# Kernel tuning notes

Hardware: AMD Instinct MI355X
Metric: run time of the kernel (lower is better)

Reference implementation:

```python
import math
import jax, jax.numpy as jnp
import numpy as np

B, T, D, NE, DS, H = 8, 1024, 768, 8, 128, 64
ROUTE_TEMP = 1.0


def setup_inputs() -> dict:
    key = jax.random.key(0)
    ks = jax.random.split(key, 32)
    rn = lambda k, shape, s=0.02: (jax.random.normal(k, shape, jnp.float32) * s)
    inp = {
        "h_seq": jax.random.normal(ks[0], (B, T, D), jnp.float32),
        "entity_keys": rn(ks[1], (NE, D)),
        "state0": rn(ks[2], (NE, DS)),
        # input_proj
        "Wi": rn(ks[3], (DS, D), 0.05), "bi": jnp.zeros((DS,), jnp.float32),
        # GRUCell (torch layout: [3*DS, DS], gate order r,z,n)
        "W_ih": rn(ks[4], (3 * DS, DS), 0.05), "W_hh": rn(ks[5], (3 * DS, DS), 0.05),
        "b_ih": rn(ks[6], (3 * DS,), 0.05), "b_hh": rn(ks[7], (3 * DS,), 0.05),
        # memory_proj
        "Wm": rn(ks[8], (D, DS), 0.05), "bm": jnp.zeros((D,), jnp.float32),
        # sequence_proj
        "Ws": rn(ks[9], (D, NE * D), 0.02), "bs": jnp.zeros((D,), jnp.float32),
        # heads: Linear(DS,H) -> GELU -> Linear(H,1)
        "Wh1": rn(ks[10], (H, DS), 0.05), "bh1": jnp.zeros((H,), jnp.float32),
        "Wh2": rn(ks[11], (1, H), 0.05), "bh2": jnp.zeros((1,), jnp.float32),
        "Wt1": rn(ks[12], (H, DS), 0.05), "bt1": jnp.zeros((H,), jnp.float32),
        "Wt2": rn(ks[13], (1, H), 0.05), "bt2": jnp.zeros((1,), jnp.float32),
        "Wv1": rn(ks[14], (H, DS), 0.05), "bv1": jnp.zeros((H,), jnp.float32),
        "Wv2": rn(ks[15], (1, H), 0.05), "bv2": jnp.zeros((1,), jnp.float32),
    }
    return inp


def _gru_cell(x, h, W_ih, W_hh, b_ih, b_hh):
    # x, h: [..., DS]; torch GRUCell semantics, gate order (r, z, n)
    gi = x @ W_ih.T + b_ih
    gh = h @ W_hh.T + b_hh
    i_r, i_z, i_n = jnp.split(gi, 3, axis=-1)
    h_r, h_z, h_n = jnp.split(gh, 3, axis=-1)
    r = jax.nn.sigmoid(i_r + h_r)
    z = jax.nn.sigmoid(i_z + h_z)
    n = jnp.tanh(i_n + r * h_n)
    return (1.0 - z) * n + z * h


def _head(s, W1, b1, W2, b2):
    # s: [B,T,NE,DS] -> logits [B,T,NE]
    hdn = jax.nn.gelu(s @ W1.T + b1, approximate=False)
    return (hdn @ W2.T + b2)[..., 0]


def reference(h_seq, entity_keys, state0, Wi, bi, W_ih, W_hh, b_ih, b_hh,
              Wm, bm, Ws, bs, Wh1, bh1, Wh2, bh2, Wt1, bt1, Wt2, bt2,
              Wv1, bv1, Wv2, bv2):
    scale = math.sqrt(D) * max(1e-4, ROUTE_TEMP)
    route_logits = jnp.einsum("btd,ed->bte", h_seq, entity_keys) / scale
    route_weights = jax.nn.softmax(route_logits, axis=-1)           # [B,T,NE]
    projected = h_seq @ Wi.T + bi                                   # [B,T,DS]
    routed = route_weights[..., None] * projected[:, :, None, :]    # [B,T,NE,DS]

    def step(state, x_t):  # state,x_t: [B,NE,DS]
        new = _gru_cell(x_t, state, W_ih, W_hh, b_ih, b_hh)
        return new, new

    init = jnp.broadcast_to(state0, (B, NE, DS))
    _, states = jax.lax.scan(step, init, routed.transpose(1, 0, 2, 3))
    state_stack = states.transpose(1, 0, 2, 3)                      # [B,T,NE,DS]

    memory_stack = state_stack @ Wm.T + bm                          # [B,T,NE,D]
    holder = _head(state_stack, Wh1, bh1, Wh2, bh2)
    tagged = _head(state_stack, Wt1, bt1, Wt2, bt2)
    visible = _head(state_stack, Wv1, bv1, Wv2, bv2)
    pooled = memory_stack.reshape(B, T, NE * D) @ Ws.T + bs         # [B,T,D]
    return pooled, memory_stack, state_stack, holder, tagged, visible, route_weights
```

## Files before the change

### kernel.cpp

```cpp
#include <hip/hip_runtime.h>
#include <hip/hip_bf16.h>

typedef unsigned short u16;
typedef unsigned int u32;
typedef __bf16 bf16x8 __attribute__((ext_vector_type(8)));
typedef float f32x4 __attribute__((ext_vector_type(4)));

#define OUT_POOLED 0
#define OUT_MEM    6291456
#define OUT_STATE  56623104
#define OUT_HOLD   65011712
#define OUT_ROUTE  65208320

#define SW(r) (((r)&7)<<4)

__device__ __forceinline__ float b2f(u16 u){ u32 v=((u32)u)<<16; float f; __builtin_memcpy(&f,&v,4); return f; }
__device__ __forceinline__ u16 f2b(float f){ __hip_bfloat16 h=__float2bfloat16(f); u16 r; __builtin_memcpy(&r,&h,2); return r; }
__device__ __forceinline__ float sigf(float x){ return __builtin_amdgcn_rcpf(1.0f+__builtin_amdgcn_exp2f(-1.4426950408889634f*x)); }
__device__ __forceinline__ float tanh_(float x){ return 1.0f-2.0f*__builtin_amdgcn_rcpf(1.0f+__builtin_amdgcn_exp2f(2.8853900817779268f*x)); }
__device__ __forceinline__ float geluf(float x){
  float z = 0.7071067811865476f*x;
  float az = __builtin_fabsf(z);
  float t = __builtin_amdgcn_rcpf(1.0f+0.3275911f*az);
  float p = t*(0.254829592f+t*(-0.284496736f+t*(1.421413741f+t*(-1.453152027f+t*1.061405429f))));
  float e = __builtin_amdgcn_exp2f(-1.4426950408889634f*az*az);
  float er = 1.0f-p*e;
  er = (z<0.0f)? -er : er;
  return 0.5f*x*(1.0f+er);
}

__global__ void k_prep(const float* __restrict__ Ws, const float* __restrict__ bs,
                       const float* __restrict__ bm, const float* __restrict__ Wm,
                       const float* __restrict__ Wh1, const float* __restrict__ bh1,
                       const float* __restrict__ Wt1, const float* __restrict__ bt1,
                       const float* __restrict__ Wv1, const float* __restrict__ bv1,
                       const float* __restrict__ Wi, const float* __restrict__ ek,
                       const float* __restrict__ Wih,
                       u16* __restrict__ wcat, float* __restrict__ bcat, float* __restrict__ bcomb,
                       u16* __restrict__ wib2, u16* __restrict__ wihb, u16* __restrict__ wmT)
{
  __shared__ float bmS[768];
  int tid = threadIdx.x;
  for(int i=tid;i<768;i+=256) bmS[i]=bm[i];
  __syncthreads();
  {
    int w = tid>>6, lane = tid&63;
    int d = blockIdx.x*4 + w;
    float acc=0.f;
    for(int e=0;e<8;e++){
      const float* row = Ws + (size_t)d*6144 + e*768;
      #pragma unroll
      for(int it=0; it<3; it++){
        int c = it*256 + lane*4;
        float4 u = *reinterpret_cast<const float4*>(row + c);
        acc += u.x*bmS[c]+u.y*bmS[c+1]+u.z*bmS[c+2]+u.w*bmS[c+3];
      }
    }
    #pragma unroll
    for(int o=32;o>0;o>>=1) acc += __shfl_down(acc,o);
    if(lane==0) bcomb[d]=bs[d]+acc;
  }
  for(int idx = blockIdx.x*256+tid; idx<381888; idx += gridDim.x*256){
    if(idx<960){
      int n=idx;
      float v;
      if(n<768) v=bm[n];
      else { int j=n-768; v = (j<64)? bh1[j] : (j<128)? bt1[j-64] : bv1[j-128]; }
      bcat[n]=v;
    } else if(idx<123840){
      int c=idx-960; int n=c>>7, k=c&127;
      float v;
      if(n<768) v=Wm[n*128+k];
      else if(n<832) v=Wh1[(n-768)*128+k];
      else if(n<896) v=Wt1[(n-832)*128+k];
      else v=Wv1[(n-896)*128+k];
      wcat[c]=f2b(v);
    } else if(idx<234432){
      int j=idx-123840; int r=j/768, k=j-r*768;
      float v = (r<128)? Wi[r*768+k] : (r<136)? ek[(r-128)*768+k] : 0.f;
      wib2[j]=f2b(v);
    } else if(idx<283584){
      int j=idx-234432;
      wihb[j]=f2b(Wih[j]);
    } else {
      int j=idx-283584; int s=j/768, d2=j-s*768;
      wmT[j]=f2b(Wm[d2*128+s]);
    }
  }
}

__global__ __launch_bounds__(256,2) void k_wcomb(const float* __restrict__ Ws, const u16* __restrict__ wmT,
                                                 u16* __restrict__ wcomb)
{
  __shared__ u16 AsU[128*104];
  __shared__ u16 BsU[128*104];
  char* AsB=(char*)AsU; char* BsB=(char*)BsU;
  int tid=threadIdx.x;
  int dt=blockIdx.x, e=blockIdx.y;
  int d0=dt*128;
  int w=tid>>6, L=tid&63, q4=L>>4, il=L&15;
  int msub=w*32;
  const f32x4 fz={0.f,0.f,0.f,0.f};
  f32x4 acc[2][8];
  #pragma unroll
  for(int tm=0;tm<2;tm++)
    #pragma unroll
    for(int tn=0;tn<8;tn++) acc[tm][tn]=fz;
  for(int kc=0;kc<8;kc++){
    __syncthreads();
    for(int it=0;it<12;it++){
      int slot=it*256+tid; int r=slot/24, c4=(slot-r*24)*4;
      float4 u=*reinterpret_cast<const float4*>(Ws + (size_t)(d0+r)*6144 + e*768 + kc*96 + c4);
      u16 v[4]={f2b(u.x),f2b(u.y),f2b(u.z),f2b(u.w)};
      uint2 p; __builtin_memcpy(&p,v,8);
      *reinterpret_cast<uint2*>(AsB + r*208 + c4*2) = p;
    }
    for(int it=0;it<6;it++){
      int slot=it*256+tid; int r=slot/12, o8=(slot-r*12)*8;
      uint4 u=*reinterpret_cast<const uint4*>(wmT + (size_t)r*768 + kc*96 + o8);
      *reinterpret_cast<uint4*>(BsB + r*208 + o8*2) = u;
    }
    __syncthreads();
    #pragma unroll
    for(int kt=0;kt<3;kt++){
      int kb=(kt*32+q4*8)*2;
      bf16x8 a0=__builtin_bit_cast(bf16x8,*reinterpret_cast<const uint4*>(AsB + (msub+il)*208 + kb));
      bf16x8 a1=__builtin_bit_cast(bf16x8,*reinterpret_cast<const uint4*>(AsB + (msub+16+il)*208 + kb));
      #pragma unroll
      for(int tn=0;tn<8;tn++){
        bf16x8 b=__builtin_bit_cast(bf16x8,*reinterpret_cast<const uint4*>(BsB + (tn*16+il)*208 + kb));
        acc[0][tn]=__builtin_amdgcn_mfma_f32_16x16x32_bf16(a0,b,acc[0][tn],0,0,0);
        acc[1][tn]=__builtin_amdgcn_mfma_f32_16x16x32_bf16(a1,b,acc[1][tn],0,0,0);
      }
    }
  }
  #pragma unroll
  for(int tm=0;tm<2;tm++){
    #pragma unroll
    for(int tn=0;tn<8;tn++){
      #pragma unroll
      for(int i=0;i<4;i++){
        int d=d0+msub+tm*16+q4*4+i;
        wcomb[d*1024 + e*128 + tn*16+il]=f2b(acc[tm][tn][i]);
      }
    }
  }
}

__global__ __launch_bounds__(256,2) void k_route(const float* __restrict__ hseq,
                                                 const u16* __restrict__ wib2, const u16* __restrict__ wihb,
                                                 const float* __restrict__ bi,
                                                 const float* __restrict__ bih, const float* __restrict__ bhh,
                                                 u16* __restrict__ gpre, float* __restrict__ out)
{
  __shared__ u16 AsU[16*768];
  __shared__ u16 BsU[15360];
  __shared__ u16 prS[16*128];
  __shared__ float lgs[16][8];
  __shared__ float wSm[16][8];
  __shared__ float biS[128];
  __shared__ float bS[384];
  char* AsB=(char*)AsU; char* BsB=(char*)BsU; char* prB=(char*)prS;
  int tid=threadIdx.x;
  int row0=blockIdx.x*16;
  {
    int r=tid>>4, c0=(tid&15)*48;
    const float* src=hseq+(size_t)(row0+r)*768+c0;
    #pragma unroll
    for(int m=0;m<12;m++){
      float4 u=*reinterpret_cast<const float4*>(src+m*4);
      u16 v[4]={f2b(u.x),f2b(u.y),f2b(u.z),f2b(u.w)};
      uint2 p; __builtin_memcpy(&p,v,8);
      int k=c0+m*4;
      *reinterpret_cast<uint2*>(AsB + r*1536 + ((k*2)^SW(r))) = p;
    }
  }
  if(tid<32){ *reinterpret_cast<float4*>(&biS[tid*4]) = *reinterpret_cast<const float4*>(bi+tid*4); }
  if(tid>=64&&tid<160){
    int j4=(tid-64)*4;
    float4 u=*reinterpret_cast<const float4*>(bih+j4);
    if(j4<256){ float4 v=*reinterpret_cast<const float4*>(bhh+j4); u.x+=v.x;u.y+=v.y;u.z+=v.z;u.w+=v.w; }
    *reinterpret_cast<float4*>(&bS[j4])=u;
  }
  int w=tid>>6, L=tid&63, q4=L>>4, il=L&15;
  int ntP=(w==0)?3:2;
  f32x4 accP[3];
  #pragma unroll
  for(int i=0;i<3;i++) accP[i]=(f32x4){0.f,0.f,0.f,0.f};
  for(int kc=0;kc<8;kc++){
    __syncthreads();
    for(int it=0;it<7;it++){
      int slot=it*256+tid;
      if(slot<1728){
        int r=slot/12, o8=(slot-r*12)*8;
        uint4 u=*reinterpret_cast<const uint4*>(wib2 + (size_t)r*768 + kc*96 + o8);
        *reinterpret_cast<uint4*>(BsB + r*208 + o8*2) = u;
      }
    }
    __syncthreads();
    #pragma unroll
    for(int kt=0;kt<3;kt++){
      int k=kc*96+kt*32+q4*8;
      bf16x8 a=__builtin_bit_cast(bf16x8,*reinterpret_cast<const uint4*>(AsB + il*1536 + ((k*2)^SW(il))));
      int kb=(kt*32+q4*8)*2;
      #pragma unroll
      for(int t3=0;t3<3;t3++){
        if(t3<ntP){
          int col=(w+t3*4)*16+il;
          bf16x8 b=__builtin_bit_cast(bf16x8,*reinterpret_cast<const uint4*>(BsB + col*208 + kb));
          accP[t3]=__builtin_amdgcn_mfma_f32_16x16x32_bf16(a,b,accP[t3],0,0,0);
        }
      }
    }
  }
  #pragma unroll
  for(int t3=0;t3<3;t3++){
    if(t3<ntP){
      int tn=w+t3*4;
      #pragma unroll
      for(int i=0;i<4;i++){
        int r=q4*4+i;
        float v=accP[t3][i];
        if(tn<8){
          int col=tn*16+il;
          *reinterpret_cast<u16*>(prB + r*256 + ((col*2)^SW(r))) = f2b(v+biS[col]);
        } else if(il<8){
          lgs[r][il]=v*(1.0f/27.712812921102035f);
        }
      }
    }
  }
  __syncthreads();
  if(tid<16){
    int r=tid;
    float l[8],m=-1e30f;
    #pragma unroll
    for(int e=0;e<8;e++){ l[e]=lgs[r][e]; m=fmaxf(m,l[e]); }
    float s=0.f;
    #pragma unroll
    for(int e=0;e<8;e++){ l[e]=__builtin_amdgcn_exp2f(1.4426950408889634f*(l[e]-m)); s+=l[e]; }
    float inv=__builtin_amdgcn_rcpf(s);
    #pragma unroll
    for(int e=0;e<8;e++){ float wv=l[e]*inv; wSm[r][e]=wv; out[OUT_ROUTE+(row0+r)*8+e]=wv; }
  }
  f32x4 accQ[6];
  #pragma unroll
  for(int i=0;i<6;i++) accQ[i]=(f32x4){0.f,0.f,0.f,0.f};
  for(int kt=0;kt<4;kt++){
    __syncthreads();
    for(int it=0;it<6;it++){
      int slot=it*256+tid;
      int r=slot>>2, qt=slot&3;
      uint4 u=*reinterpret_cast<const uint4*>(wihb + (size_t)r*128 + kt*32 + qt*8);
      *reinterpret_cast<uint4*>(BsB + r*80 + qt*16) = u;
    }
    __syncthreads();
    int kb=(kt*32+q4*8)*2;
    bf16x8 a=__builtin_bit_cast(bf16x8,*reinterpret_cast<const uint4*>(prB + il*256 + (kb^SW(il))));
    #pragma unroll
    for(int t6=0;t6<6;t6++){
      int col=(w+t6*4)*16+il;
      bf16x8 b=__builtin_bit_cast(bf16x8,*reinterpret_cast<const uint4*>(BsB + col*80 + q4*16));
      accQ[t6]=__builtin_amdgcn_mfma_f32_16x16x32_bf16(a,b,accQ[t6],0,0,0);
    }
  }
  float* qS=(float*)AsU;
  #pragma unroll
  for(int t6=0;t6<6;t6++){
    int col=(w+t6*4)*16+il;
    #pragma unroll
    for(int i=0;i<4;i++) qS[(q4*4+i)*384+col]=accQ[t6][i];
  }
  __syncthreads();
  {
    int ch=tid&127, hh=tid>>7;
    float b0=bS[ch], b1=bS[128+ch], b2=bS[256+ch];
    #pragma unroll 1
    for(int r=0;r<16;r++){
      float q0=qS[r*384+ch], q1=qS[r*384+128+ch], q2=qS[r*384+256+ch];
      u16* dst=gpre+(size_t)(row0+r)*4096;
      #pragma unroll
      for(int j=0;j<4;j++){
        int e=(hh+j*2)&7;
        float wv=wSm[r][e];
        u16 ov[4]={f2b(wv*q0+b0),f2b(wv*q1+b1),f2b(wv*q2+b2),0};
        uint2 o; __builtin_memcpy(&o,ov,8);
        *reinterpret_cast<uint2*>(dst + (e*128+ch)*4)=o;
      }
    }
  }
}

#define SCAN_SYNC asm volatile("s_waitcnt lgkmcnt(0)\n\ts_barrier" ::: "memory")

#define SCAN_STEP(BUF,NXT,P,DOLOAD)                                                         \
  {                                                                                         \
    bf16x8 af[4];                                                                           \
    _Pragma("unroll")                                                                       \
    for(int kt=0;kt<4;kt++)                                                                 \
      af[kt]=__builtin_bit_cast(bf16x8, *reinterpret_cast<const uint4*>(&hbf[BUF][il>>2][kt*32+q4*8])); \
    u16 cw[4];                                                                              \
    __builtin_memcpy(cw,&gv[P],8);                                                          \
    if(DOLOAD){                                                                             \
      gv[P]=*reinterpret_cast<const uint2*>(gp);                                            \
      gp+=4096;                                                                             \
    }                                                                                       \
    f32x4 acc0={0.f,0.f,0.f,0.f}, acc1={0.f,0.f,0.f,0.f}, acc2={0.f,0.f,0.f,0.f};           \
    _Pragma("unroll")                                                                       \
    for(int kt=0;kt<4;kt++){                                                                \
      acc0=__builtin_amdgcn_mfma_f32_16x16x32_bf16(af[kt],bfr0[kt],acc0,0,0,0);             \
      acc1=__builtin_amdgcn_mfma_f32_16x16x32_bf16(af[kt],bfr1[kt],acc1,0,0,0);             \
      acc2=__builtin_amdgcn_mfma_f32_16x16x32_bf16(af[kt],bfr2[kt],acc2,0,0,0);             \
    }                                                                                       \
    {                                                                                       \
      float r=sigf(acc0[0]+b2f(cw[0]));                                                     \
      float z=sigf(acc1[0]+b2f(cw[1]));                                                     \
      float n=tanh_(b2f(cw[2])+r*(acc2[0]+bhhn));                                           \
      float hn=n+z*(hp-n);                                                                  \
      hp=hn;                                                                                \
      u16 hb=f2b(hn);                                                                       \
      hbf[NXT][q4][ch]=hb;                                                                  \
      *sbase=hb;                                                                            \
    }                                                                                       \
    sbase += 1024;                                                                          \
    SCAN_SYNC;                                                                              \
  }

__global__ __launch_bounds__(512,1) void k_scan(const float* __restrict__ Whh, const float* __restrict__ bhh,
                                                const float* __restrict__ state0,
                                                const u16* __restrict__ gpre, u16* __restrict__ shadow)
{
  __shared__ u16 hbf[2][4][144];
  int tid=threadIdx.x;
  int w=tid>>6, L=tid&63, q4=L>>4, il=L&15;
  int blk=blockIdx.x;
  int b=blk>>1, e0=(blk&1)*4;
  int ch=w*16+il;
  bf16x8 bfr0[4], bfr1[4], bfr2[4];
  #pragma unroll
  for(int kt=0; kt<4; kt++){
    u16 t0[8],t1[8],t2[8];
    #pragma unroll
    for(int j=0;j<8;j++){
      t0[j]=f2b(Whh[(0*128+ch)*128 + kt*32 + q4*8 + j]);
      t1[j]=f2b(Whh[(1*128+ch)*128 + kt*32 + q4*8 + j]);
      t2[j]=f2b(Whh[(2*128+ch)*128 + kt*32 + q4*8 + j]);
    }
    __builtin_memcpy(&bfr0[kt],t0,16);
    __builtin_memcpy(&bfr1[kt],t1,16);
    __builtin_memcpy(&bfr2[kt],t2,16);
  }
  float bhhn = bhh[256+ch];
  float hp = state0[(e0+q4)*128+ch];
  {
    int cc=tid>>7, chh=tid&127;
    hbf[0][cc][chh]=f2b(state0[(e0+cc)*128+chh]);
  }
  const u16* gp = gpre + (size_t)b*1024*4096 + ((e0+q4)*128+ch)*4;
  u16* sbase = shadow + ((size_t)b*1024*8 + (e0+q4))*128 + ch;
  uint2 gv[4];
  #pragma unroll
  for(int p=0;p<4;p++){
    gv[p]=*reinterpret_cast<const uint2*>(gp);
    gp+=4096;
  }
  SCAN_SYNC;
  #pragma unroll 1
  for(int t2=0;t2<255;t2++){
    SCAN_STEP(0,1,0,1)
    SCAN_STEP(1,0,1,1)
    SCAN_STEP(0,1,2,1)
    SCAN_STEP(1,0,3,1)
  }
  SCAN_STEP(0,1,0,0)
  SCAN_STEP(1,0,1,0)
  SCAN_STEP(0,1,2,0)
  SCAN_STEP(1,0,3,0)
}

__global__ __launch_bounds__(256) void k_expand(const u16* __restrict__ sh, float* __restrict__ o)
{
  int idx=(blockIdx.x*256+threadIdx.x)*4;
  uint2 u=*reinterpret_cast<const uint2*>(sh+idx);
  float4 f;
  f.x=b2f((u16)(u.x&0xffffu)); f.y=b2f((u16)(u.x>>16));
  f.z=b2f((u16)(u.y&0xffffu)); f.w=b2f((u16)(u.y>>16));
  *reinterpret_cast<float4*>(o+idx)=f;
}

__global__ __launch_bounds__(256) void k_mem(const u16* __restrict__ state, const u16* __restrict__ wcat,
                                             const float* __restrict__ bcat,
                                             float* __restrict__ memout, u16* __restrict__ hdn)
{
  __shared__ u16 As[128][136];
  __shared__ u16 Bs[96][136];
  int tid=threadIdx.x;
  int bx=blockIdx.x, ny=blockIdx.y;
  for(int it=0;it<8;it++){
    int v=it*256+tid; int r=v>>4, c8=(v&15)*8;
    *reinterpret_cast<uint4*>(&As[r][c8]) = *reinterpret_cast<const uint4*>(state + (bx*128+r)*128 + c8);
  }
  for(int it=0;it<6;it++){
    int v=it*256+tid; int r=v>>4, c8=(v&15)*8;
    *reinterpret_cast<uint4*>(&Bs[r][c8]) = *reinterpret_cast<const uint4*>(wcat + (ny*96+r)*128 + c8);
  }
  __syncthreads();
  int w=tid>>6, L=tid&63, q4=L>>4, il=L&15;
  int msub=w*32;
  bf16x8 af[2][4];
  #pragma unroll
  for(int tm=0;tm<2;tm++)
    #pragma unroll
    for(int kt=0;kt<4;kt++)
      af[tm][kt]=__builtin_bit_cast(bf16x8,*reinterpret_cast<const uint4*>(&As[msub+tm*16+il][kt*32+q4*8]));
  const f32x4 fz = {0.f,0.f,0.f,0.f};
  f32x4 acc[2][6];
  #pragma unroll
  for(int tm=0;tm<2;tm++){
    #pragma unroll
    for(int tn=0;tn<6;tn++) acc[tm][tn]=fz;
  }
  #pragma unroll
  for(int tn=0;tn<6;tn++){
    bf16x8 bf[4];
    #pragma unroll
    for(int kt=0;kt<4;kt++)
      bf[kt]=__builtin_bit_cast(bf16x8,*reinterpret_cast<const uint4*>(&Bs[tn*16+il][kt*32+q4*8]));
    #pragma unroll
    for(int tm=0;tm<2;tm++){
      #pragma unroll
      for(int kt=0;kt<4;kt++)
        acc[tm][tn]=__builtin_amdgcn_mfma_f32_16x16x32_bf16(af[tm][kt],bf[kt],acc[tm][tn],0,0,0);
    }
  }
  #pragma unroll
  for(int tm=0;tm<2;tm++){
    #pragma unroll
    for(int tn=0;tn<6;tn++){
      int col=ny*96+tn*16+il;
      float bias=bcat[col];
      #pragma unroll
      for(int i=0;i<4;i++){
        int row=bx*128+msub+tm*16+q4*4+i;
        float val=acc[tm][tn][i]+bias;
        if(ny<8) memout[row*768+col]=val;
        else hdn[row*192+(col-768)]=f2b(geluf(val));
      }
    }
  }
}

__global__ __launch_bounds__(256) void k_pool(const u16* __restrict__ state, const u16* __restrict__ wcomb,
                                              const float* __restrict__ bcomb, float* __restrict__ pooled)
{
  __shared__ u16 As[128][136];
  __shared__ u16 Bs[96][136];
  int tid=threadIdx.x;
  int bx=blockIdx.x, ny=blockIdx.y;
  int w=tid>>6, L=tid&63, q4=L>>4, il=L&15;
  int msub=w*32;
  const f32x4 fz = {0.f,0.f,0.f,0.f};
  f32x4 acc[2][6];
  #pragma unroll
  for(int tm=0;tm<2;tm++){
    #pragma unroll
    for(int tn=0;tn<6;tn++) acc[tm][tn]=fz;
  }
  for(int kc=0;kc<8;kc++){
    __syncthreads();
    for(int it=0;it<8;it++){
      int v=it*256+tid; int r=v>>4, c8=(v&15)*8;
      *reinterpret_cast<uint4*>(&As[r][c8]) = *reinterpret_cast<const uint4*>(state + (bx*128+r)*1024 + kc*128 + c8);
    }
    for(int it=0;it<6;it++){
      int v=it*256+tid; int r=v>>4, c8=(v&15)*8;
      *reinterpret_cast<uint4*>(&Bs[r][c8]) = *reinterpret_cast<const uint4*>(wcomb + (ny*96+r)*1024 + kc*128 + c8);
    }
    __syncthreads();
    bf16x8 af[2][4];
    #pragma unroll
    for(int tm=0;tm<2;tm++)
      #pragma unroll
      for(int kt=0;kt<4;kt++)
        af[tm][kt]=__builtin_bit_cast(bf16x8,*reinterpret_cast<const uint4*>(&As[msub+tm*16+il][kt*32+q4*8]));
    #pragma unroll
    for(int tn=0;tn<6;tn++){
      bf16x8 bf[4];
      #pragma unroll
      for(int kt=0;kt<4;kt++)
        bf[kt]=__builtin_bit_cast(bf16x8,*reinterpret_cast<const uint4*>(&Bs[tn*16+il][kt*32+q4*8]));
      #pragma unroll
      for(int tm=0;tm<2;tm++){
        #pragma unroll
        for(int kt=0;kt<4;kt++)
          acc[tm][tn]=__builtin_amdgcn_mfma_f32_16x16x32_bf16(af[tm][kt],bf[kt],acc[tm][tn],0,0,0);
      }
    }
  }
  #pragma unroll
  for(int tm=0;tm<2;tm++){
    #pragma unroll
    for(int tn=0;tn<6;tn++){
      int col=ny*96+tn*16+il;
      float bias=bcomb[col];
      #pragma unroll
      for(int i=0;i<4;i++){
        int row=bx*128+msub+tm*16+q4*4+i;
        pooled[row*768+col]=acc[tm][tn][i]+bias;
      }
    }
  }
}

__global__ __launch_bounds__(256) void k_heads(const u16* __restrict__ hdn,
                                               const float* __restrict__ Wh2, const float* __restrict__ bh2,
                                               const float* __restrict__ Wt2, const float* __restrict__ bt2,
                                               const float* __restrict__ Wv2, const float* __restrict__ bv2,
                                               float* __restrict__ out)
{
  int oid=blockIdx.x*256+threadIdx.x;
  int row=oid&65535, head=oid>>16;
  const float* w2 = (head==0)?Wh2:(head==1)?Wt2:Wv2;
  float b2 = ((head==0)?bh2:(head==1)?bt2:bv2)[0];
  float acc=0.f;
  const u16* src = hdn + row*192 + head*64;
  for(int j0=0;j0<64;j0+=8){
    uint4 hu=*reinterpret_cast<const uint4*>(src+j0);
    u16 hs[8]; __builtin_memcpy(hs,&hu,16);
    #pragma unroll
    for(int j=0;j<8;j++) acc+=b2f(hs[j])*w2[j0+j];
  }
  out[OUT_HOLD + head*65536 + row]=acc+b2;
}

extern "C" void kernel_launch(void* const* d_in, const int* in_sizes, int n_in,
                              void* d_out, int out_size, void* d_ws, size_t ws_size,
                              hipStream_t stream)
{
  const float* hseq=(const float*)d_in[0];
  const float* ek  =(const float*)d_in[1];
  const float* st0 =(const float*)d_in[2];
  const float* Wi  =(const float*)d_in[3];
  const float* bi  =(const float*)d_in[4];
  const float* Wih =(const float*)d_in[5];
  const float* Whh =(const float*)d_in[6];
  const float* bih =(const float*)d_in[7];
  const float* bhh =(const float*)d_in[8];
  const float* Wm  =(const float*)d_in[9];
  const float* bm  =(const float*)d_in[10];
  const float* Ws  =(const float*)d_in[11];
  const float* bs  =(const float*)d_in[12];
  const float* Wh1 =(const float*)d_in[13];
  const float* bh1 =(const float*)d_in[14];
  const float* Wh2 =(const float*)d_in[15];
  const float* bh2 =(const float*)d_in[16];
  const float* Wt1 =(const float*)d_in[17];
  const float* bt1 =(const float*)d_in[18];
  const float* Wt2 =(const float*)d_in[19];
  const float* bt2 =(const float*)d_in[20];
  const float* Wv1 =(const float*)d_in[21];
  const float* bv1 =(const float*)d_in[22];
  const float* Wv2 =(const float*)d_in[23];
  const float* bv2 =(const float*)d_in[24];
  float* out=(float*)d_out;
  char* ws=(char*)d_ws;
  u16*  gpre  =(u16*)ws;
  u16*  wcomb =(u16*)(ws+67108864);
  float* bcomb=(float*)(ws+68681728);
  u16*  wcat  =(u16*)(ws+68684800);
  float* bcat =(float*)(ws+68930560);
  u16*  shadow=(u16*)(ws+68934400);
  u16*  wib2  =(u16*)(ws+85711616);
  u16*  wihb  =(u16*)(ws+85932800);
  u16*  wmT   =(u16*)(ws+86031104);
  u16*  hdn   =(u16*)ws;

  hipLaunchKernelGGL(k_prep, dim3(192), dim3(256), 0, stream,
                     Ws,bs,bm,Wm,Wh1,bh1,Wt1,bt1,Wv1,bv1,Wi,ek,Wih,wcat,bcat,bcomb,wib2,wihb,wmT);
  hipLaunchKernelGGL(k_wcomb, dim3(6,8), dim3(256), 0, stream, Ws,wmT,wcomb);
  hipLaunchKernelGGL(k_route, dim3(512), dim3(256), 0, stream, hseq,wib2,wihb,bi,bih,bhh,gpre,out);
  hipLaunchKernelGGL(k_scan, dim3(16), dim3(512), 0, stream, Whh,bhh,st0,gpre,shadow);
  hipLaunchKernelGGL(k_expand, dim3(8192), dim3(256), 0, stream, shadow,out+OUT_STATE);
  hipLaunchKernelGGL(k_mem, dim3(512,10), dim3(256), 0, stream, shadow,wcat,bcat,out+OUT_MEM,hdn);
  hipLaunchKernelGGL(k_pool, dim3(64,8), dim3(256), 0, stream, shadow,wcomb,bcomb,out+OUT_POOLED);
  hipLaunchKernelGGL(k_heads, dim3(768), dim3(256), 0, stream, hdn,Wh2,bh2,Wt2,bt2,Wv2,bv2,out);
}
```

Before: 859.8 us.

## Halve scan block to 4 waves with two channel groups each, fuse fp32 state store

```diff
diff --git a/kernel.cpp b/kernel.cpp
--- a/kernel.cpp
+++ b/kernel.cpp
@@ -299,69 +299,88 @@
     _Pragma("unroll")                                                                       \
     for(int kt=0;kt<4;kt++)                                                                 \
       af[kt]=__builtin_bit_cast(bf16x8, *reinterpret_cast<const uint4*>(&hbf[BUF][il>>2][kt*32+q4*8])); \
-    u16 cw[4];                                                                              \
-    __builtin_memcpy(cw,&gv[P],8);                                                          \
+    u16 cwa[4], cwb[4];                                                                     \
+    __builtin_memcpy(cwa,&gva[P],8);                                                        \
+    __builtin_memcpy(cwb,&gvb[P],8);                                                        \
     if(DOLOAD){                                                                             \
-      gv[P]=*reinterpret_cast<const uint2*>(gp);                                            \
+      gva[P]=*reinterpret_cast<const uint2*>(gp);                                           \
+      gvb[P]=*reinterpret_cast<const uint2*>(gp+256);                                       \
       gp+=4096;                                                                             \
     }                                                                                       \
-    f32x4 acc0={0.f,0.f,0.f,0.f}, acc1={0.f,0.f,0.f,0.f}, acc2={0.f,0.f,0.f,0.f};           \
+    f32x4 ac[2][3];                                                                         \
+    _Pragma("unroll")                                                                       \
+    for(int cg=0;cg<2;cg++){                                                                \
+      _Pragma("unroll")                                                                     \
+      for(int g=0;g<3;g++) ac[cg][g]=(f32x4){0.f,0.f,0.f,0.f};                              \
+    }                                                                                       \
     _Pragma("unroll")                                                                       \
     for(int kt=0;kt<4;kt++){                                                                \
-      acc0=__builtin_amdgcn_mfma_f32_16x16x32_bf16(af[kt],bfr0[kt],acc0,0,0,0);             \
-      acc1=__builtin_amdgcn_mfma_f32_16x16x32_bf16(af[kt],bfr1[kt],acc1,0,0,0);             \
-      acc2=__builtin_amdgcn_mfma_f32_16x16x32_bf16(af[kt],bfr2[kt],acc2,0,0,0);             \
+      _Pragma("unroll")                                                                     \
+      for(int cg=0;cg<2;cg++){                                                              \
+        _Pragma("unroll")                                                                   \
+        for(int g=0;g<3;g++)                                                                \
+          ac[cg][g]=__builtin_amdgcn_mfma_f32_16x16x32_bf16(af[kt],bfr[cg][g][kt],ac[cg][g],0,0,0); \
+      }                                                                                     \
     }                                                                                       \
     {                                                                                       \
-      float r=sigf(acc0[0]+b2f(cw[0]));                                                     \
-      float z=sigf(acc1[0]+b2f(cw[1]));                                                     \
-      float n=tanh_(b2f(cw[2])+r*(acc2[0]+bhhn));                                           \
-      float hn=n+z*(hp-n);                                                                  \
-      hp=hn;                                                                                \
-      u16 hb=f2b(hn);                                                                       \
-      hbf[NXT][q4][ch]=hb;                                                                  \
-      *sbase=hb;                                                                            \
+      float r0=sigf(ac[0][0][0]+b2f(cwa[0]));                                               \
+      float z0=sigf(ac[0][1][0]+b2f(cwa[1]));                                               \
+      float n0=tanh_(b2f(cwa[2])+r0*(ac[0][2][0]+bhhn0));                                   \
+      float h0=n0+z0*(hp0-n0);  hp0=h0;                                                     \
+      float r1=sigf(ac[1][0][0]+b2f(cwb[0]));                                               \
+      float z1=sigf(ac[1][1][0]+b2f(cwb[1]));                                               \
+      float n1=tanh_(b2f(cwb[2])+r1*(ac[1][2][0]+bhhn1));                                   \
+      float h1=n1+z1*(hp1-n1);  hp1=h1;                                                     \
+      u16 hb0=f2b(h0), hb1=f2b(h1);                                                         \
+      hbf[NXT][q4][ch0]=hb0;                                                                \
+      hbf[NXT][q4][ch1]=hb1;                                                                \
+      sbase[0]=hb0; sbase[64]=hb1;                                                          \
+      obase[0]=h0;  obase[64]=h1;                                                           \
     }                                                                                       \
-    sbase += 1024;                                                                          \
+    sbase += 1024; obase += 1024;                                                           \
     SCAN_SYNC;                                                                              \
   }
 
-__global__ __launch_bounds__(512,1) void k_scan(const float* __restrict__ Whh, const float* __restrict__ bhh,
+__global__ __launch_bounds__(256,1) void k_scan(const float* __restrict__ Whh, const float* __restrict__ bhh,
                                                 const float* __restrict__ state0,
-                                                const u16* __restrict__ gpre, u16* __restrict__ shadow)
+                                                const u16* __restrict__ gpre, u16* __restrict__ shadow,
+                                                float* __restrict__ outstate)
 {
   __shared__ u16 hbf[2][4][144];
   int tid=threadIdx.x;
   int w=tid>>6, L=tid&63, q4=L>>4, il=L&15;
   int blk=blockIdx.x;
   int b=blk>>1, e0=(blk&1)*4;
-  int ch=w*16+il;
-  bf16x8 bfr0[4], bfr1[4], bfr2[4];
-  #pragma unroll
-  for(int kt=0; kt<4; kt++){
-    u16 t0[8],t1[8],t2[8];
-    #pragma unroll
-    for(int j=0;j<8;j++){
-      t0[j]=f2b(Whh[(0*128+ch)*128 + kt*32 + q4*8 + j]);
-      t1[j]=f2b(Whh[(1*128+ch)*128 + kt*32 + q4*8 + j]);
-      t2[j]=f2b(Whh[(2*128+ch)*128 + kt*32 + q4*8 + j]);
-    }
-    __builtin_memcpy(&bfr0[kt],t0,16);
-    __builtin_memcpy(&bfr1[kt],t1,16);
-    __builtin_memcpy(&bfr2[kt],t2,16);
-  }
-  float bhhn = bhh[256+ch];
-  float hp = state0[(e0+q4)*128+ch];
-  {
-    int cc=tid>>7, chh=tid&127;
-    hbf[0][cc][chh]=f2b(state0[(e0+cc)*128+chh]);
-  }
-  const u16* gp = gpre + (size_t)b*1024*4096 + ((e0+q4)*128+ch)*4;
-  u16* sbase = shadow + ((size_t)b*1024*8 + (e0+q4))*128 + ch;
-  uint2 gv[4];
+  int ch0=w*16+il, ch1=64+ch0;
+  bf16x8 bfr[2][3][4];
+  #pragma unroll
+  for(int cg=0; cg<2; cg++){
+    #pragma unroll
+    for(int g=0; g<3; g++){
+      #pragma unroll
+      for(int kt=0; kt<4; kt++){
+        u16 t[8];
+        #pragma unroll
+        for(int j=0;j<8;j++)
+          t[j]=f2b(Whh[(size_t)(g*128 + cg*64 + ch0)*128 + kt*32 + q4*8 + j]);
+        __builtin_memcpy(&bfr[cg][g][kt],t,16);
+      }
+    }
+  }
+  float bhhn0 = bhh[256+ch0], bhhn1 = bhh[256+ch1];
+  float hp0 = state0[(e0+q4)*128+ch0], hp1 = state0[(e0+q4)*128+ch1];
+  for(int idx=tid; idx<512; idx+=256){
+    int m=idx>>7, c=idx&127;
+    hbf[0][m][c]=f2b(state0[(e0+m)*128+c]);
+  }
+  const u16* gp = gpre + (size_t)b*1024*4096 + ((e0+q4)*128+ch0)*4;
+  u16* sbase = shadow + ((size_t)b*8192 + (e0+q4))*128 + ch0;
+  float* obase = outstate + ((size_t)b*8192 + (e0+q4))*128 + ch0;
+  uint2 gva[4], gvb[4];
   #pragma unroll
   for(int p=0;p<4;p++){
-    gv[p]=*reinterpret_cast<const uint2*>(gp);
+    gva[p]=*reinterpret_cast<const uint2*>(gp);
+    gvb[p]=*reinterpret_cast<const uint2*>(gp+256);
     gp+=4096;
   }
   SCAN_SYNC;
@@ -376,16 +395,6 @@
   SCAN_STEP(1,0,1,0)
   SCAN_STEP(0,1,2,0)
   SCAN_STEP(1,0,3,0)
-}
-
-__global__ __launch_bounds__(256) void k_expand(const u16* __restrict__ sh, float* __restrict__ o)
-{
-  int idx=(blockIdx.x*256+threadIdx.x)*4;
-  uint2 u=*reinterpret_cast<const uint2*>(sh+idx);
-  float4 f;
-  f.x=b2f((u16)(u.x&0xffffu)); f.y=b2f((u16)(u.x>>16));
-  f.z=b2f((u16)(u.y&0xffffu)); f.w=b2f((u16)(u.y>>16));
-  *reinterpret_cast<float4*>(o+idx)=f;
 }
 
 __global__ __launch_bounds__(256) void k_mem(const u16* __restrict__ state, const u16* __restrict__ wcat,
@@ -579,8 +588,7 @@
                      Ws,bs,bm,Wm,Wh1,bh1,Wt1,bt1,Wv1,bv1,Wi,ek,Wih,wcat,bcat,bcomb,wib2,wihb,wmT);
   hipLaunchKernelGGL(k_wcomb, dim3(6,8), dim3(256), 0, stream, Ws,wmT,wcomb);
   hipLaunchKernelGGL(k_route, dim3(512), dim3(256), 0, stream, hseq,wib2,wihb,bi,bih,bhh,gpre,out);
-  hipLaunchKernelGGL(k_scan, dim3(16), dim3(512), 0, stream, Whh,bhh,st0,gpre,shadow);
-  hipLaunchKernelGGL(k_expand, dim3(8192), dim3(256), 0, stream, shadow,out+OUT_STATE);
+  hipLaunchKernelGGL(k_scan, dim3(16), dim3(256), 0, stream, Whh,bhh,st0,gpre,shadow,out+OUT_STATE);
   hipLaunchKernelGGL(k_mem, dim3(512,10), dim3(256), 0, stream, shadow,wcat,bcat,out+OUT_MEM,hdn);
   hipLaunchKernelGGL(k_pool, dim3(64,8), dim3(256), 0, stream, shadow,wcomb,bcomb,out+OUT_POOLED);
   hipLaunchKernelGGL(k_heads, dim3(768), dim3(256), 0, stream, hdn,Wh2,bh2,Wt2,bt2,Wv2,bv2,out);
```

Result: slower. 922.8 us (+7.3%).
